# Kernel optimization log

Hardware: AMD Instinct MI355X
Metric: run time of the kernel (lower is better)

Reference implementation:

```python
import jax, jax.numpy as jnp
import numpy as np

N, E, B = 32768, 524288, 256
IN_N, IN_E, HID, L = 6, 2, 64, 3
STATE_DIM, ACT_DIM = 16, 2
MLP1, MLP2 = 256, 256
EPS_AGG, EPS_BN = 1e-6, 1e-5


def setup_inputs() -> dict:
    key = jax.random.key(0)
    ks = iter(jax.random.split(key, 48))
    def nrm(shape, scale=0.05):
        return jax.random.normal(next(ks), shape, dtype=jnp.float32) * scale
    inp = {
        'h': jax.random.normal(next(ks), (N, IN_N), dtype=jnp.float32),
        # edge features are inverted (1/e) in the model, so keep them positive
        'e_feat': jax.random.uniform(next(ks), (E, IN_E), dtype=jnp.float32, minval=0.5, maxval=1.5),
        'src': jax.random.randint(next(ks), (E,), 0, N, dtype=jnp.int32),
        'dst': jax.random.randint(next(ks), (E,), 0, N, dtype=jnp.int32),
        'graph_ids': jnp.sort(jax.random.randint(next(ks), (N,), 0, B, dtype=jnp.int32)),
        'state': jax.random.normal(next(ks), (B, STATE_DIM), dtype=jnp.float32),
        'action': jax.random.normal(next(ks), (B, ACT_DIM), dtype=jnp.float32),
        'emb_h_W': nrm((IN_N, HID)), 'emb_h_b': jnp.zeros((HID,), jnp.float32),
        'emb_e_W': nrm((IN_E, HID)), 'emb_e_b': jnp.zeros((HID,), jnp.float32),
        'A_W': nrm((L, HID, HID)), 'A_b': jnp.zeros((L, HID), jnp.float32),
        'B_W': nrm((L, HID, HID)), 'B_b': jnp.zeros((L, HID), jnp.float32),
        'C_W': nrm((L, HID, HID)), 'C_b': jnp.zeros((L, HID), jnp.float32),
        'D_W': nrm((L, HID, HID)), 'D_b': jnp.zeros((L, HID), jnp.float32),
        'E_W': nrm((L, HID, HID)), 'E_b': jnp.zeros((L, HID), jnp.float32),
        'bn_h_g': jnp.ones((L, HID), jnp.float32), 'bn_h_beta': jnp.zeros((L, HID), jnp.float32),
        'bn_e_g': jnp.ones((L, HID), jnp.float32), 'bn_e_beta': jnp.zeros((L, HID), jnp.float32),
        'l1_W': nrm((HID + STATE_DIM + ACT_DIM, MLP1)), 'l1_b': jnp.zeros((MLP1,), jnp.float32),
        'l2_W': nrm((MLP1, MLP2)), 'l2_b': jnp.zeros((MLP2,), jnp.float32),
        'l3_W': nrm((MLP2, 1)), 'l3_b': jnp.zeros((1,), jnp.float32),
    }
    return inp


def _batch_norm(x, g, b):
    # BatchNorm1d in training mode: normalize over the node/edge axis
    mu = jnp.mean(x, axis=0)
    var = jnp.var(x, axis=0)
    return g * (x - mu) * jax.lax.rsqrt(var + EPS_BN) + b


def _forward(h, e_feat, src, dst, graph_ids, state, action,
             emb_h_W, emb_h_b, emb_e_W, emb_e_b,
             A_W, A_b, B_W, B_b, C_W, C_b, D_W, D_b, E_W, E_b,
             bn_h_g, bn_h_beta, bn_e_g, bn_e_beta,
             l1_W, l1_b, l2_W, l2_b, l3_W, l3_b):
    e = 1.0 / e_feat                       # model feeds reciprocal edge features
    h = h @ emb_h_W + emb_h_b              # [N, HID]
    e = e @ emb_e_W + emb_e_b              # [E, HID]
    n = h.shape[0]
    for l in range(L):
        Ah = h @ A_W[l] + A_b[l]
        Bh = h @ B_W[l] + B_b[l]
        Dh = h @ D_W[l] + D_b[l]
        Eh = h @ E_W[l] + E_b[l]
        Ce = e @ C_W[l] + C_b[l]
        e_hat = Ce + Dh[src] + Eh[dst]     # edge update [E, HID]
        sigma = jax.nn.sigmoid(e_hat)
        num = jax.ops.segment_sum(sigma * Bh[src], dst, num_segments=n)
        den = jax.ops.segment_sum(sigma, dst, num_segments=n)
        h_new = Ah + num / (den + EPS_AGG)
        h = h + jax.nn.relu(_batch_norm(h_new, bn_h_g[l], bn_h_beta[l]))  # residual
        e = e + jax.nn.relu(_batch_norm(e_hat, bn_e_g[l], bn_e_beta[l]))
    # mean readout per graph
    counts = jax.ops.segment_sum(jnp.ones((n,), h.dtype), graph_ids, num_segments=B)
    hg = jax.ops.segment_sum(h, graph_ids, num_segments=B) / jnp.maximum(counts, 1.0)[:, None]
    x = jnp.concatenate([hg, state, action], axis=-1)
    x = jax.nn.relu(x @ l1_W + l1_b)
    x = jax.nn.relu(x @ l2_W + l2_b)
    return x @ l3_W + l3_b                 # [B, 1]


def reference(h, e_feat, src, dst, graph_ids, state, action,
              emb_h_W, emb_h_b, emb_e_W, emb_e_b,
              A_W, A_b, B_W, B_b, C_W, C_b, D_W, D_b, E_W, E_b,
              bn_h_g, bn_h_beta, bn_e_g, bn_e_beta,
              l1_W, l1_b, l2_W, l2_b, l3_W, l3_b):
    return _forward(h, e_feat, src, dst, graph_ids, state, action,
                    emb_h_W, emb_h_b, emb_e_W, emb_e_b,
                    A_W, A_b, B_W, B_b, C_W, C_b, D_W, D_b, E_W, E_b,
                    bn_h_g, bn_h_beta, bn_e_g, bn_e_beta,
                    l1_W, l1_b, l2_W, l2_b, l3_W, l3_b)
```

## Files before the change

### kernel.cpp

```cpp
#include <hip/hip_runtime.h>
#include <math.h>

#define NN 32768
#define NE 524288
#define NB 256
#define HID 64
#define NL 3
#define EPS_AGG 1e-6f
#define EPS_BN 1e-5f
#define AGG_BLOCKS 2048
#define EF_BLOCKS 2048
#define NG_BLOCKS 2048
#define NBANK 16
#define S_ESC 4096
#define S_ESH 4160
#define S_HSC 4224
#define S_HSH 4288

typedef _Float16 h16;
typedef h16 h16x8 __attribute__((ext_vector_type(8)));
typedef h16 h16x4 __attribute__((ext_vector_type(4)));
typedef float f32x4 __attribute__((ext_vector_type(4)));

#define MFMA16(a, b, c) __builtin_amdgcn_mfma_f32_16x16x32_f16(a, b, c, 0, 0, 0)


__global__ void k_zero4(float4* __restrict__ p, long n4) {
    long t = (long)blockIdx.x * blockDim.x + threadIdx.x;
    long stride = (long)gridDim.x * blockDim.x;
    float4 z = {0.f, 0.f, 0.f, 0.f};
    for (; t < n4; t += stride) p[t] = z;
}


__global__ void k_hist(const int* __restrict__ dst, int* __restrict__ hist) {
    int i = blockIdx.x * blockDim.x + threadIdx.x;
    atomicAdd(&hist[dst[i]], 1);
}

__global__ void k_scan(const int* __restrict__ hist, int* __restrict__ rowptr,
                       int* __restrict__ cursor) {
    __shared__ int part[1024];
    int t = threadIdx.x;
    int loc[32];
    int base = t * 32, sum = 0;
#pragma unroll
    for (int k = 0; k < 32; ++k) { loc[k] = hist[base + k]; sum += loc[k]; }
    part[t] = sum;
    __syncthreads();
    for (int off = 1; off < 1024; off <<= 1) {
        int v = (t >= off) ? part[t - off] : 0;
        __syncthreads();
        part[t] += v;
        __syncthreads();
    }
    int ex = part[t] - sum;
#pragma unroll
    for (int k = 0; k < 32; ++k) {
        rowptr[base + k] = ex; cursor[base + k] = ex; ex += loc[k];
    }
    if (t == 1023) rowptr[NN] = ex;
}

__global__ void k_scatter(const int* __restrict__ src, const int* __restrict__ dst,
                          int* __restrict__ cursor, int* __restrict__ eperm,
                          int* __restrict__ src_s, int* __restrict__ dst_s) {
    int i = blockIdx.x * blockDim.x + threadIdx.x;
    int d = dst[i];
    int pos = atomicAdd(&cursor[d], 1);
    eperm[pos] = i;
    src_s[pos] = src[i];
    dst_s[pos] = d;
}


__global__ void k_ghist(const int* __restrict__ gid, int* __restrict__ ghist) {
    int i = blockIdx.x * blockDim.x + threadIdx.x;
    atomicAdd(&ghist[gid[i]], 1);
}

__global__ void k_gscan(const int* __restrict__ ghist, int* __restrict__ grp) {
    __shared__ int part[256];
    int t = threadIdx.x;
    int v = ghist[t];
    part[t] = v;
    __syncthreads();
    for (int off = 1; off < 256; off <<= 1) {
        int u = (t >= off) ? part[t - off] : 0;
        __syncthreads();
        part[t] += u;
        __syncthreads();
    }
    grp[t + 1] = part[t];
    if (t == 0) grp[0] = 0;
}


__global__ void k_embed_h(const float* __restrict__ hin, const float* __restrict__ W,
                          const float* __restrict__ b, float* __restrict__ out,
                          h16* __restrict__ out16) {
    int tid = blockIdx.x * blockDim.x + threadIdx.x;
    int i = tid >> 6, j = tid & 63;
    float acc = b[j];
#pragma unroll
    for (int k = 0; k < 6; ++k) acc += hin[i * 6 + k] * W[k * 64 + j];
    out[tid] = acc;
    out16[tid] = (h16)acc;
}

__global__ void k_embed_e_perm(const float* __restrict__ ef, const int* __restrict__ eperm,
                               const float* __restrict__ W, const float* __restrict__ b,
                               h16* __restrict__ out) {
    int t = blockIdx.x * blockDim.x + threadIdx.x;
    int pos = t >> 3, j0 = (t & 7) * 8;
    int i = eperm[pos];
    float r0 = 1.0f / ef[i * 2 + 0];
    float r1 = 1.0f / ef[i * 2 + 1];
    float4 b0 = *(const float4*)&b[j0],      b1 = *(const float4*)&b[j0 + 4];
    float4 w00 = *(const float4*)&W[j0],     w01 = *(const float4*)&W[j0 + 4];
    float4 w10 = *(const float4*)&W[64 + j0], w11 = *(const float4*)&W[64 + j0 + 4];
    h16x8 o;
    o[0] = (h16)(b0.x + r0 * w00.x + r1 * w10.x);
    o[1] = (h16)(b0.y + r0 * w00.y + r1 * w10.y);
    o[2] = (h16)(b0.z + r0 * w00.z + r1 * w10.z);
    o[3] = (h16)(b0.w + r0 * w00.w + r1 * w10.w);
    o[4] = (h16)(b1.x + r0 * w01.x + r1 * w11.x);
    o[5] = (h16)(b1.y + r0 * w01.y + r1 * w11.y);
    o[6] = (h16)(b1.z + r0 * w01.z + r1 * w11.z);
    o[7] = (h16)(b1.w + r0 * w01.w + r1 * w11.w);
    *(h16x8*)&out[(size_t)pos * 64 + j0] = o;
}


__global__ void k_node_gemm(const h16* __restrict__ X,
                            const float* __restrict__ AW, const float* __restrict__ Ab,
                            const float* __restrict__ BW, const float* __restrict__ Bb,
                            const float* __restrict__ DW, const float* __restrict__ Db,
                            const float* __restrict__ EW, const float* __restrict__ Eb,
                            float* __restrict__ Ah, h16* __restrict__ Bh,
                            h16* __restrict__ Dh, h16* __restrict__ Eh) {
    __shared__ float tr[4][16][68];
    int lane = threadIdx.x & 63, wid = threadIdx.x >> 6;
    int wg = blockIdx.x * 4 + wid;
    int m = wg & 3, tile = wg >> 2;
    int ar = lane & 15, ak = (lane >> 4) * 8;
    int r = lane >> 2, c0 = (lane & 3) * 16;
    const float* W  = (m == 0) ? AW : (m == 1) ? BW : (m == 2) ? DW : EW;
    const float* Bb_ = (m == 0) ? Ab : (m == 1) ? Bb : (m == 2) ? Db : Eb;
    h16x8 wb0[4], wb1[4];
    float bias[4];
#pragma unroll
    for (int ct = 0; ct < 4; ++ct) {
        int col = ct * 16 + ar;
#pragma unroll
        for (int k = 0; k < 8; ++k) {
            wb0[ct][k] = (h16)W[(ak + k) * 64 + col];
            wb1[ct][k] = (h16)W[(32 + ak + k) * 64 + col];
        }
        bias[ct] = Bb_[col];
    }
    int row0 = tile * 16;
    h16x8 a0 = *(const h16x8*)&X[(size_t)(row0 + ar) * 64 + ak];
    h16x8 a1 = *(const h16x8*)&X[(size_t)(row0 + ar) * 64 + 32 + ak];
#pragma unroll
    for (int ct = 0; ct < 4; ++ct) {
        float bv = bias[ct];
        f32x4 acc = (f32x4){bv, bv, bv, bv};
        acc = MFMA16(a0, wb0[ct], acc);
        acc = MFMA16(a1, wb1[ct], acc);
#pragma unroll
        for (int j = 0; j < 4; ++j)
            tr[wid][(lane >> 4) * 4 + j][ct * 16 + ar] = acc[j];
    }
    if (m == 0) {
#pragma unroll
        for (int j = 0; j < 4; ++j)
            *(float4*)&Ah[(size_t)(row0 + r) * 64 + c0 + j * 4] =
                *(float4*)&tr[wid][r][c0 + j * 4];
    } else {
        h16* out = (m == 1) ? Bh : (m == 2) ? Dh : Eh;
        h16x8 o0, o1;
#pragma unroll
        for (int j = 0; j < 8; ++j) {
            o0[j] = (h16)tr[wid][r][c0 + j];
            o1[j] = (h16)tr[wid][r][c0 + 8 + j];
        }
        *(h16x8*)&out[(size_t)(row0 + r) * 64 + c0] = o0;
        *(h16x8*)&out[(size_t)(row0 + r) * 64 + c0 + 8] = o1;
    }
}


template <int MODE>
__global__ void k_edge_fwd(const h16* __restrict__ e, h16* __restrict__ ewr,
                           const float* __restrict__ CW, const float* __restrict__ Cb,
                           const h16* __restrict__ Dh, const h16* __restrict__ Eh,
                           const int* __restrict__ src_s, const int* __restrict__ dst_s,
                           h16* __restrict__ ehat, const float* __restrict__ stats) {
    __shared__ float tr[4][16][68];
    int lane = threadIdx.x & 63, wid = threadIdx.x >> 6;
    int ar = lane & 15, ak = (lane >> 4) * 8;
    int r = lane >> 2, c0 = (lane & 3) * 16;
    int sb = ((blockIdx.x & 7) << 8) | (blockIdx.x >> 3);
    h16x8 wb0[4], wb1[4];
    float bias[4];
#pragma unroll
    for (int ct = 0; ct < 4; ++ct) {
        int col = ct * 16 + ar;
#pragma unroll
        for (int k = 0; k < 8; ++k) {
            wb0[ct][k] = (h16)CW[(ak + k) * 64 + col];
            wb1[ct][k] = (h16)CW[(32 + ak + k) * 64 + col];
        }
        bias[ct] = Cb[col];
    }
    float sc0[8], sh0[8], sc1[8], sh1[8];
    if (MODE != 0) {
#pragma unroll
        for (int k = 0; k < 8; ++k) {
            sc0[k] = stats[S_ESC + ak + k];      sh0[k] = stats[S_ESH + ak + k];
            sc1[k] = stats[S_ESC + 32 + ak + k]; sh1[k] = stats[S_ESH + 32 + ak + k];
        }
    }
    for (int tile = sb * 4 + wid; tile < NE / 16; tile += EF_BLOCKS * 4) {
        int e0 = tile * 16;
        size_t fbase = (size_t)(e0 + ar) * 64;
        h16x8 a0, a1;
        if (MODE == 0) {
            a0 = *(const h16x8*)&e[fbase + ak];
            a1 = *(const h16x8*)&e[fbase + 32 + ak];
        } else {
            h16x8 ep0 = *(const h16x8*)&e[fbase + ak];
            h16x8 ep1 = *(const h16x8*)&e[fbase + 32 + ak];
            h16x8 eh0 = *(const h16x8*)&ehat[fbase + ak];
            h16x8 eh1 = *(const h16x8*)&ehat[fbase + 32 + ak];
#pragma unroll
            for (int k = 0; k < 8; ++k) {
                a0[k] = (h16)((float)ep0[k] + fmaxf(0.f, (float)eh0[k] * sc0[k] + sh0[k]));
                a1[k] = (h16)((float)ep1[k] + fmaxf(0.f, (float)eh1[k] * sc1[k] + sh1[k]));
            }
            if (MODE == 1) {
                *(h16x8*)&ewr[fbase + ak] = a0;
                *(h16x8*)&ewr[fbase + 32 + ak] = a1;
            }
        }
        int er = e0 + r;
        int s = src_s[er], d = dst_s[er];
#pragma unroll
        for (int ct = 0; ct < 4; ++ct) {
            float bv = bias[ct];
            f32x4 acc = (f32x4){bv, bv, bv, bv};
            acc = MFMA16(a0, wb0[ct], acc);
            acc = MFMA16(a1, wb1[ct], acc);
#pragma unroll
            for (int j = 0; j < 4; ++j)
                tr[wid][(lane >> 4) * 4 + j][ct * 16 + ar] = acc[j];
        }
        h16x8 d0 = *(const h16x8*)&Dh[(size_t)s * 64 + c0];
        h16x8 d1 = *(const h16x8*)&Dh[(size_t)s * 64 + c0 + 8];
        h16x8 g0 = *(const h16x8*)&Eh[(size_t)d * 64 + c0];
        h16x8 g1 = *(const h16x8*)&Eh[(size_t)d * 64 + c0 + 8];
        h16x8 o0, o1;
#pragma unroll
        for (int j = 0; j < 8; ++j) {
            o0[j] = (h16)(tr[wid][r][c0 + j] + (float)d0[j] + (float)g0[j]);
            o1[j] = (h16)(tr[wid][r][c0 + 8 + j] + (float)d1[j] + (float)g1[j]);
        }
        *(h16x8*)&ehat[(size_t)er * 64 + c0] = o0;
        *(h16x8*)&ehat[(size_t)er * 64 + c0 + 8] = o1;
    }
}


__global__ void k_agg_node(const h16* __restrict__ ehat, const h16* __restrict__ Bh,
                           const int* __restrict__ src_s, const int* __restrict__ rowptr,
                           const float* __restrict__ Ah, float* __restrict__ hnew,
                           float* __restrict__ stats) {
    __shared__ float red[256];
    int lane = threadIdx.x & 63, wid = threadIdx.x >> 6;
    int wglob = blockIdx.x * 4 + wid;
    float esum = 0.f, esq = 0.f, hsum = 0.f, hsq = 0.f;
    for (int d = wglob; d < NN; d += AGG_BLOCKS * 4) {
        int begin = rowptr[d], end = rowptr[d + 1];
        float accn = 0.f, accd = 0.f;
        int p = begin;
        for (; p + 8 <= end; p += 8) {
            int   ss[8]; float eh[8], bh[8];
#pragma unroll
            for (int q = 0; q < 8; ++q) ss[q] = src_s[p + q];
#pragma unroll
            for (int q = 0; q < 8; ++q) eh[q] = (float)ehat[(size_t)(p + q) * 64 + lane];
#pragma unroll
            for (int q = 0; q < 8; ++q) bh[q] = (float)Bh[(size_t)ss[q] * 64 + lane];
#pragma unroll
            for (int q = 0; q < 8; ++q) {
                float ev = eh[q];
                esum += ev; esq += ev * ev;
                float sg = 1.0f / (1.0f + __expf(-ev));
                accn += sg * bh[q]; accd += sg;
            }
        }
        if (p + 4 <= end) {
            int   ss[4]; float eh[4], bh[4];
#pragma unroll
            for (int q = 0; q < 4; ++q) ss[q] = src_s[p + q];
#pragma unroll
            for (int q = 0; q < 4; ++q) eh[q] = (float)ehat[(size_t)(p + q) * 64 + lane];
#pragma unroll
            for (int q = 0; q < 4; ++q) bh[q] = (float)Bh[(size_t)ss[q] * 64 + lane];
#pragma unroll
            for (int q = 0; q < 4; ++q) {
                float ev = eh[q];
                esum += ev; esq += ev * ev;
                float sg = 1.0f / (1.0f + __expf(-ev));
                accn += sg * bh[q]; accd += sg;
            }
            p += 4;
        }
        for (; p < end; ++p) {
            float ev = (float)ehat[(size_t)p * 64 + lane];
            int s = src_s[p];
            float bv = (float)Bh[(size_t)s * 64 + lane];
            esum += ev; esq += ev * ev;
            float sg = 1.0f / (1.0f + __expf(-ev));
            accn += sg * bv; accd += sg;
        }
        float hv = Ah[(size_t)d * 64 + lane] + accn / (accd + EPS_AGG);
        hnew[(size_t)d * 64 + lane] = hv;
        hsum += hv; hsq += hv * hv;
    }
    float vals[4] = {esum, esq, hsum, hsq};
    int bank = blockIdx.x & (NBANK - 1);
#pragma unroll
    for (int s2 = 0; s2 < 4; ++s2) {
        red[wid * 64 + lane] = vals[s2];
        __syncthreads();
        if (wid == 0)
            atomicAdd(&stats[bank * 256 + s2 * 64 + lane],
                      red[lane] + red[64 + lane] + red[128 + lane] + red[192 + lane]);
        __syncthreads();
    }
}


__global__ void k_finstats2(float* __restrict__ stats, const float* __restrict__ eg,
                            const float* __restrict__ eb, const float* __restrict__ hgm,
                            const float* __restrict__ hbt) {
    int t = threadIdx.x;
    float s1 = 0.f, s2 = 0.f;
    if (t < 64) {
#pragma unroll
        for (int b = 0; b < NBANK; ++b) {
            s1 += stats[b * 256 + t];
            s2 += stats[b * 256 + 64 + t];
        }
    } else {
        int j = t - 64;
#pragma unroll
        for (int b = 0; b < NBANK; ++b) {
            s1 += stats[b * 256 + 128 + j];
            s2 += stats[b * 256 + 192 + j];
        }
    }
    float o1, o2; int i1, i2;
    if (t < 64) {
        float mu = s1 / (float)NE;
        float var = s2 / (float)NE - mu * mu;
        float rs = rsqrtf(var + EPS_BN);
        float g = eg[t];
        o1 = g * rs; o2 = eb[t] - g * mu * rs;
        i1 = S_ESC + t; i2 = S_ESH + t;
    } else {
        int j = t - 64;
        float mu = s1 / (float)NN;
        float var = s2 / (float)NN - mu * mu;
        float rs = rsqrtf(var + EPS_BN);
        float g = hgm[j];
        o1 = g * rs; o2 = hbt[j] - g * mu * rs;
        i1 = S_HSC + j; i2 = S_HSH + j;
    }
    __syncthreads();
    for (int i = t; i < NBANK * 256; i += 128) stats[i] = 0.f;
    stats[i1] = o1; stats[i2] = o2;
}


__global__ void k_hbn_apply(float* __restrict__ h, h16* __restrict__ h16buf,
                            const float* __restrict__ hnew,
                            const float* __restrict__ stats) {
    int t = blockIdx.x * blockDim.x + threadIdx.x;
    int j4 = t & 15;
    float4 s = ((const float4*)(stats + S_HSC))[j4];
    float4 b = ((const float4*)(stats + S_HSH))[j4];
    float4 v = ((const float4*)hnew)[t];
    float4 x = ((const float4*)h)[t];
    x.x += fmaxf(0.f, v.x * s.x + b.x);
    x.y += fmaxf(0.f, v.y * s.y + b.y);
    x.z += fmaxf(0.f, v.z * s.z + b.z);
    x.w += fmaxf(0.f, v.w * s.w + b.w);
    ((float4*)h)[t] = x;
    h16x4 o;
    o[0] = (h16)x.x; o[1] = (h16)x.y; o[2] = (h16)x.z; o[3] = (h16)x.w;
    *(h16x4*)&h16buf[(size_t)t * 4] = o;
}


__global__ void k_graph_mean(const float* __restrict__ h, const int* __restrict__ grp,
                             float* __restrict__ hg) {
    int lane = threadIdx.x & 63, wid = threadIdx.x >> 6;
    int g = blockIdx.x * 4 + wid;
    int begin = grp[g], end = grp[g + 1];
    float acc = 0.f;
    int i = begin;
    for (; i + 4 <= end; i += 4) {
        float a0 = h[(size_t)(i + 0) * 64 + lane];
        float a1 = h[(size_t)(i + 1) * 64 + lane];
        float a2 = h[(size_t)(i + 2) * 64 + lane];
        float a3 = h[(size_t)(i + 3) * 64 + lane];
        acc += (a0 + a1) + (a2 + a3);
    }
    for (; i < end; ++i) acc += h[(size_t)i * 64 + lane];
    float cnt = (float)(end - begin);
    hg[g * 64 + lane] = acc / fmaxf(cnt, 1.0f);
}


__global__ void k_mlp1(const float* __restrict__ hg, const float* __restrict__ st,
                       const float* __restrict__ ac, const float* __restrict__ W,
                       const float* __restrict__ b, float* __restrict__ out) {
    __shared__ float x[82];
    int bidx = blockIdx.x, t = threadIdx.x;
    if (t < 64) x[t] = hg[bidx * 64 + t];
    else if (t < 80) x[t] = st[bidx * 16 + (t - 64)];
    else if (t < 82) x[t] = ac[bidx * 2 + (t - 80)];
    __syncthreads();
    float acc = b[t];
#pragma unroll
    for (int k = 0; k < 82; ++k) acc += x[k] * W[k * 256 + t];
    out[bidx * 256 + t] = fmaxf(acc, 0.f);
}

__global__ void k_mlp2(const float* __restrict__ xin, const float* __restrict__ W,
                       const float* __restrict__ b, float* __restrict__ out) {
    __shared__ float x[256];
    int bidx = blockIdx.x, t = threadIdx.x;
    x[t] = xin[bidx * 256 + t];
    __syncthreads();
    float acc = b[t];
#pragma unroll 8
    for (int k = 0; k < 256; ++k) acc += x[k] * W[k * 256 + t];
    out[bidx * 256 + t] = fmaxf(acc, 0.f);
}

__global__ void k_mlp3(const float* __restrict__ xin, const float* __restrict__ W,
                       const float* __restrict__ b, float* __restrict__ out) {
    int t = threadIdx.x;
    float acc = b[0];
#pragma unroll 8
    for (int k = 0; k < 256; ++k) acc += xin[t * 256 + k] * W[k];
    out[t] = acc;
}


extern "C" void kernel_launch(void* const* d_in, const int* in_sizes, int n_in,
                              void* d_out, int out_size, void* d_ws, size_t ws_size,
                              hipStream_t stream) {
    const float* in_h   = (const float*)d_in[0];
    const float* e_feat = (const float*)d_in[1];
    const int*   src    = (const int*)d_in[2];
    const int*   dst    = (const int*)d_in[3];
    const int*   gid    = (const int*)d_in[4];
    const float* state  = (const float*)d_in[5];
    const float* action = (const float*)d_in[6];
    const float* embhW  = (const float*)d_in[7];
    const float* embhb  = (const float*)d_in[8];
    const float* embeW  = (const float*)d_in[9];
    const float* embeb  = (const float*)d_in[10];
    const float* A_W = (const float*)d_in[11]; const float* A_b = (const float*)d_in[12];
    const float* B_W = (const float*)d_in[13]; const float* B_b = (const float*)d_in[14];
    const float* C_W = (const float*)d_in[15]; const float* C_b = (const float*)d_in[16];
    const float* D_W = (const float*)d_in[17]; const float* D_b = (const float*)d_in[18];
    const float* E_W = (const float*)d_in[19]; const float* E_b = (const float*)d_in[20];
    const float* bnhg = (const float*)d_in[21]; const float* bnhb = (const float*)d_in[22];
    const float* bneg = (const float*)d_in[23]; const float* bneb = (const float*)d_in[24];
    const float* l1W = (const float*)d_in[25]; const float* l1b = (const float*)d_in[26];
    const float* l2W = (const float*)d_in[27]; const float* l2b = (const float*)d_in[28];
    const float* l3W = (const float*)d_in[29]; const float* l3b = (const float*)d_in[30];

    char* base = (char*)d_ws;
    size_t off = 0;
    auto alloc = [&](size_t bytes) {
        off = (off + 255) & ~(size_t)255;
        void* p = base + off; off += bytes; return p;
    };
    h16*   e_s    = (h16*)  alloc((size_t)NE * 64 * 2);
    h16*   ehat   = (h16*)  alloc((size_t)NE * 64 * 2);
    float* h      = (float*)alloc((size_t)NN * 64 * 4);
    h16*   h16buf = (h16*)  alloc((size_t)NN * 64 * 2);
    float* Ah     = (float*)alloc((size_t)NN * 64 * 4);
    float* hnew   = (float*)alloc((size_t)NN * 64 * 4);
    h16*   Bh     = (h16*)  alloc((size_t)NN * 64 * 2);
    h16*   Dh     = (h16*)  alloc((size_t)NN * 64 * 2);
    h16*   Eh     = (h16*)  alloc((size_t)NN * 64 * 2);
    float* stats  = (float*)alloc((NBANK * 256 + 512) * 4);
    float* hg     = (float*)alloc((size_t)NB * 64 * 4);
    float* x1     = (float*)alloc((size_t)NB * 256 * 4);
    float* x2     = (float*)alloc((size_t)NB * 256 * 4);
    int*   eperm  = (int*)  alloc((size_t)NE * 4);
    int*   src_s  = (int*)  alloc((size_t)NE * 4);
    int*   dst_s  = (int*)  alloc((size_t)NE * 4);
    int*   hist   = (int*)  alloc((size_t)NN * 4);
    int*   ghist  = (int*)  alloc(256 * 4);
    int*   rowptr = (int*)  alloc((size_t)(NN + 1) * 4);
    int*   cursor = (int*)  alloc((size_t)NN * 4);
    int*   grp    = (int*)  alloc((size_t)(NB + 1) * 4);
    size_t need = off;

    if (ws_size < need) return;

    k_zero4<<<33, 256, 0, stream>>>((float4*)hist, ((long)NN * 4 + 256 * 4) / 16);
    k_hist<<<NE / 256, 256, 0, stream>>>(dst, hist);
    k_scan<<<1, 1024, 0, stream>>>(hist, rowptr, cursor);
    k_scatter<<<NE / 256, 256, 0, stream>>>(src, dst, cursor, eperm, src_s, dst_s);
    k_ghist<<<NN / 256, 256, 0, stream>>>(gid, ghist);
    k_gscan<<<1, 256, 0, stream>>>(ghist, grp);

    k_embed_h<<<(NN * 64) / 256, 256, 0, stream>>>(in_h, embhW, embhb, h, h16buf);
    k_embed_e_perm<<<(NE * 8) / 256, 256, 0, stream>>>(e_feat, eperm, embeW, embeb, e_s);

    k_zero4<<<4, 256, 0, stream>>>((float4*)stats, (NBANK * 256) / 4);
    for (int l = 0; l < NL; ++l) {
        k_node_gemm<<<NG_BLOCKS, 256, 0, stream>>>(h16buf,
                                                   A_W + l * 4096, A_b + l * 64,
                                                   B_W + l * 4096, B_b + l * 64,
                                                   D_W + l * 4096, D_b + l * 64,
                                                   E_W + l * 4096, E_b + l * 64,
                                                   Ah, Bh, Dh, Eh);
        if (l == 0)
            k_edge_fwd<0><<<EF_BLOCKS, 256, 0, stream>>>(e_s, nullptr,
                C_W + l * 4096, C_b + l * 64, Dh, Eh, src_s, dst_s, ehat, stats);
        else if (l == 1)
            k_edge_fwd<1><<<EF_BLOCKS, 256, 0, stream>>>(e_s, e_s,
                C_W + l * 4096, C_b + l * 64, Dh, Eh, src_s, dst_s, ehat, stats);
        else
            k_edge_fwd<2><<<EF_BLOCKS, 256, 0, stream>>>(e_s, nullptr,
                C_W + l * 4096, C_b + l * 64, Dh, Eh, src_s, dst_s, ehat, stats);
        k_agg_node<<<AGG_BLOCKS, 256, 0, stream>>>(ehat, Bh, src_s, rowptr, Ah, hnew, stats);
        k_finstats2<<<1, 128, 0, stream>>>(stats, bneg + l * 64, bneb + l * 64,
                                           bnhg + l * 64, bnhb + l * 64);
        k_hbn_apply<<<NN / 16, 256, 0, stream>>>(h, h16buf, hnew, stats);
    }

    k_graph_mean<<<NB / 4, 256, 0, stream>>>(h, grp, hg);

    k_mlp1<<<NB, 256, 0, stream>>>(hg, state, action, l1W, l1b, x1);
    k_mlp2<<<NB, 256, 0, stream>>>(x1, l2W, l2b, x2);
    k_mlp3<<<1, NB, 0, stream>>>(x2, l3W, l3b, (float*)d_out);
}
```

Before: 497.8 us.

## Fuse edge embedding into first edge layer, fuse MLP head, remap agg nodes

```diff
diff --git a/kernel.cpp b/kernel.cpp
--- a/kernel.cpp
+++ b/kernel.cpp
@@ -106,29 +106,6 @@
     for (int k = 0; k < 6; ++k) acc += hin[i * 6 + k] * W[k * 64 + j];
     out[tid] = acc;
     out16[tid] = (h16)acc;
-}
-
-__global__ void k_embed_e_perm(const float* __restrict__ ef, const int* __restrict__ eperm,
-                               const float* __restrict__ W, const float* __restrict__ b,
-                               h16* __restrict__ out) {
-    int t = blockIdx.x * blockDim.x + threadIdx.x;
-    int pos = t >> 3, j0 = (t & 7) * 8;
-    int i = eperm[pos];
-    float r0 = 1.0f / ef[i * 2 + 0];
-    float r1 = 1.0f / ef[i * 2 + 1];
-    float4 b0 = *(const float4*)&b[j0],      b1 = *(const float4*)&b[j0 + 4];
-    float4 w00 = *(const float4*)&W[j0],     w01 = *(const float4*)&W[j0 + 4];
-    float4 w10 = *(const float4*)&W[64 + j0], w11 = *(const float4*)&W[64 + j0 + 4];
-    h16x8 o;
-    o[0] = (h16)(b0.x + r0 * w00.x + r1 * w10.x);
-    o[1] = (h16)(b0.y + r0 * w00.y + r1 * w10.y);
-    o[2] = (h16)(b0.z + r0 * w00.z + r1 * w10.z);
-    o[3] = (h16)(b0.w + r0 * w00.w + r1 * w10.w);
-    o[4] = (h16)(b1.x + r0 * w01.x + r1 * w11.x);
-    o[5] = (h16)(b1.y + r0 * w01.y + r1 * w11.y);
-    o[6] = (h16)(b1.z + r0 * w01.z + r1 * w11.z);
-    o[7] = (h16)(b1.w + r0 * w01.w + r1 * w11.w);
-    *(h16x8*)&out[(size_t)pos * 64 + j0] = o;
 }
 
 
@@ -196,7 +173,9 @@
                            const float* __restrict__ CW, const float* __restrict__ Cb,
                            const h16* __restrict__ Dh, const h16* __restrict__ Eh,
                            const int* __restrict__ src_s, const int* __restrict__ dst_s,
-                           h16* __restrict__ ehat, const float* __restrict__ stats) {
+                           h16* __restrict__ ehat, const float* __restrict__ stats,
+                           const float* __restrict__ ef, const int* __restrict__ eperm,
+                           const float* __restrict__ eW, const float* __restrict__ eb) {
     __shared__ float tr[4][16][68];
     int lane = threadIdx.x & 63, wid = threadIdx.x >> 6;
     int ar = lane & 15, ak = (lane >> 4) * 8;
@@ -215,7 +194,15 @@
         bias[ct] = Cb[col];
     }
     float sc0[8], sh0[8], sc1[8], sh1[8];
-    if (MODE != 0) {
+    float be0[8], w00[8], w10[8], be1[8], w01[8], w11[8];
+    if (MODE == 0) {
+#pragma unroll
+        for (int k = 0; k < 8; ++k) {
+            int c1 = ak + k, c2 = 32 + ak + k;
+            be0[k] = eb[c1]; w00[k] = eW[c1]; w10[k] = eW[64 + c1];
+            be1[k] = eb[c2]; w01[k] = eW[c2]; w11[k] = eW[64 + c2];
+        }
+    } else {
 #pragma unroll
         for (int k = 0; k < 8; ++k) {
             sc0[k] = stats[S_ESC + ak + k];      sh0[k] = stats[S_ESH + ak + k];
@@ -227,8 +214,16 @@
         size_t fbase = (size_t)(e0 + ar) * 64;
         h16x8 a0, a1;
         if (MODE == 0) {
-            a0 = *(const h16x8*)&e[fbase + ak];
-            a1 = *(const h16x8*)&e[fbase + 32 + ak];
+            int ie = eperm[e0 + ar];
+            float r0 = 1.0f / ef[ie * 2 + 0];
+            float r1 = 1.0f / ef[ie * 2 + 1];
+#pragma unroll
+            for (int k = 0; k < 8; ++k) {
+                a0[k] = (h16)(be0[k] + r0 * w00[k] + r1 * w10[k]);
+                a1[k] = (h16)(be1[k] + r0 * w01[k] + r1 * w11[k]);
+            }
+            *(h16x8*)&ewr[fbase + ak] = a0;
+            *(h16x8*)&ewr[fbase + 32 + ak] = a1;
         } else {
             h16x8 ep0 = *(const h16x8*)&e[fbase + ak];
             h16x8 ep1 = *(const h16x8*)&e[fbase + 32 + ak];
@@ -278,9 +273,11 @@
                            float* __restrict__ stats) {
     __shared__ float red[256];
     int lane = threadIdx.x & 63, wid = threadIdx.x >> 6;
-    int wglob = blockIdx.x * 4 + wid;
+    int sb = ((blockIdx.x & 7) << 8) | (blockIdx.x >> 3);
+    int w = sb * 4 + wid;
     float esum = 0.f, esq = 0.f, hsum = 0.f, hsq = 0.f;
-    for (int d = wglob; d < NN; d += AGG_BLOCKS * 4) {
+    int dlo = w * 4;
+    for (int d = dlo; d < dlo + 4; ++d) {
         int begin = rowptr[d], end = rowptr[d + 1];
         float accn = 0.f, accd = 0.f;
         int p = begin;
@@ -425,40 +422,35 @@
 }
 
 
-__global__ void k_mlp1(const float* __restrict__ hg, const float* __restrict__ st,
-                       const float* __restrict__ ac, const float* __restrict__ W,
-                       const float* __restrict__ b, float* __restrict__ out) {
-    __shared__ float x[82];
-    int bidx = blockIdx.x, t = threadIdx.x;
-    if (t < 64) x[t] = hg[bidx * 64 + t];
-    else if (t < 80) x[t] = st[bidx * 16 + (t - 64)];
-    else if (t < 82) x[t] = ac[bidx * 2 + (t - 80)];
+__global__ void k_mlp(const float* __restrict__ hg, const float* __restrict__ st,
+                      const float* __restrict__ ac,
+                      const float* __restrict__ W1, const float* __restrict__ b1,
+                      const float* __restrict__ W2, const float* __restrict__ b2,
+                      const float* __restrict__ W3, const float* __restrict__ b3,
+                      float* __restrict__ out) {
+    __shared__ float xin[88];
+    __shared__ float y[256];
+    __shared__ float red4[4];
+    int g = blockIdx.x, t = threadIdx.x;
+    if (t < 64) xin[t] = hg[g * 64 + t];
+    else if (t < 80) xin[t] = st[g * 16 + (t - 64)];
+    else if (t < 82) xin[t] = ac[g * 2 + (t - 80)];
     __syncthreads();
-    float acc = b[t];
-#pragma unroll
-    for (int k = 0; k < 82; ++k) acc += x[k] * W[k * 256 + t];
-    out[bidx * 256 + t] = fmaxf(acc, 0.f);
-}
-
-__global__ void k_mlp2(const float* __restrict__ xin, const float* __restrict__ W,
-                       const float* __restrict__ b, float* __restrict__ out) {
-    __shared__ float x[256];
-    int bidx = blockIdx.x, t = threadIdx.x;
-    x[t] = xin[bidx * 256 + t];
+    float acc = b1[t];
+#pragma unroll 2
+    for (int k = 0; k < 82; ++k) acc += xin[k] * W1[k * 256 + t];
+    y[t] = fmaxf(acc, 0.f);
     __syncthreads();
-    float acc = b[t];
+    acc = b2[t];
 #pragma unroll 8
-    for (int k = 0; k < 256; ++k) acc += x[k] * W[k * 256 + t];
-    out[bidx * 256 + t] = fmaxf(acc, 0.f);
-}
-
-__global__ void k_mlp3(const float* __restrict__ xin, const float* __restrict__ W,
-                       const float* __restrict__ b, float* __restrict__ out) {
-    int t = threadIdx.x;
-    float acc = b[0];
-#pragma unroll 8
-    for (int k = 0; k < 256; ++k) acc += xin[t * 256 + k] * W[k];
-    out[t] = acc;
+    for (int k = 0; k < 256; ++k) acc += y[k] * W2[k * 256 + t];
+    float xv = fmaxf(acc, 0.f);
+    float p = xv * W3[t];
+#pragma unroll
+    for (int o = 32; o > 0; o >>= 1) p += __shfl_down(p, o);
+    if ((t & 63) == 0) red4[t >> 6] = p;
+    __syncthreads();
+    if (t == 0) out[g] = red4[0] + red4[1] + red4[2] + red4[3] + b3[0];
 }
 
 
@@ -504,8 +496,6 @@
     h16*   Eh     = (h16*)  alloc((size_t)NN * 64 * 2);
     float* stats  = (float*)alloc((NBANK * 256 + 512) * 4);
     float* hg     = (float*)alloc((size_t)NB * 64 * 4);
-    float* x1     = (float*)alloc((size_t)NB * 256 * 4);
-    float* x2     = (float*)alloc((size_t)NB * 256 * 4);
     int*   eperm  = (int*)  alloc((size_t)NE * 4);
     int*   src_s  = (int*)  alloc((size_t)NE * 4);
     int*   dst_s  = (int*)  alloc((size_t)NE * 4);
@@ -526,7 +516,6 @@
     k_gscan<<<1, 256, 0, stream>>>(ghist, grp);
 
     k_embed_h<<<(NN * 64) / 256, 256, 0, stream>>>(in_h, embhW, embhb, h, h16buf);
-    k_embed_e_perm<<<(NE * 8) / 256, 256, 0, stream>>>(e_feat, eperm, embeW, embeb, e_s);
 
     k_zero4<<<4, 256, 0, stream>>>((float4*)stats, (NBANK * 256) / 4);
     for (int l = 0; l < NL; ++l) {
@@ -537,14 +526,17 @@
                                                    E_W + l * 4096, E_b + l * 64,
                                                    Ah, Bh, Dh, Eh);
         if (l == 0)
-            k_edge_fwd<0><<<EF_BLOCKS, 256, 0, stream>>>(e_s, nullptr,
-                C_W + l * 4096, C_b + l * 64, Dh, Eh, src_s, dst_s, ehat, stats);
+            k_edge_fwd<0><<<EF_BLOCKS, 256, 0, stream>>>(e_s, e_s,
+                C_W + l * 4096, C_b + l * 64, Dh, Eh, src_s, dst_s, ehat, stats,
+                e_feat, eperm, embeW, embeb);
         else if (l == 1)
             k_edge_fwd<1><<<EF_BLOCKS, 256, 0, stream>>>(e_s, e_s,
-                C_W + l * 4096, C_b + l * 64, Dh, Eh, src_s, dst_s, ehat, stats);
+                C_W + l * 4096, C_b + l * 64, Dh, Eh, src_s, dst_s, ehat, stats,
+                e_feat, eperm, embeW, embeb);
         else
             k_edge_fwd<2><<<EF_BLOCKS, 256, 0, stream>>>(e_s, nullptr,
-                C_W + l * 4096, C_b + l * 64, Dh, Eh, src_s, dst_s, ehat, stats);
+                C_W + l * 4096, C_b + l * 64, Dh, Eh, src_s, dst_s, ehat, stats,
+                e_feat, eperm, embeW, embeb);
         k_agg_node<<<AGG_BLOCKS, 256, 0, stream>>>(ehat, Bh, src_s, rowptr, Ah, hnew, stats);
         k_finstats2<<<1, 128, 0, stream>>>(stats, bneg + l * 64, bneb + l * 64,
                                            bnhg + l * 64, bnhb + l * 64);
@@ -553,7 +545,6 @@
 
     k_graph_mean<<<NB / 4, 256, 0, stream>>>(h, grp, hg);
 
-    k_mlp1<<<NB, 256, 0, stream>>>(hg, state, action, l1W, l1b, x1);
-    k_mlp2<<<NB, 256, 0, stream>>>(x1, l2W, l2b, x2);
-    k_mlp3<<<1, NB, 0, stream>>>(x2, l3W, l3b, (float*)d_out);
-}
+    k_mlp<<<NB, 256, 0, stream>>>(hg, state, action, l1W, l1b, l2W, l2b, l3W, l3b,
+                                  (float*)d_out);
+}
```

New measurement: 514.8 us. +3.4%, slower.
